# Optimization experiments

Measured on AMD Instinct MI355X. Metric: run time of the kernel, lower is better.

## Reference

```python
import jax, jax.numpy as jnp
import numpy as np

N_NODES = 50000
N_EDGES = 800000
VOCAB = 4096
EMB = 128
HID = 128


def glorot(key, shape):
    limit = float(np.sqrt(6.0 / (shape[0] + shape[1])))
    return jax.random.uniform(key, shape, jnp.float32, -limit, limit)


def setup_inputs() -> dict:
    key = jax.random.key(0)
    k = jax.random.split(key, 6)
    x = jax.random.randint(k[0], (N_NODES, 1), 0, VOCAB, dtype=jnp.int64)
    edge_index = jax.random.randint(k[1], (2, N_EDGES), 0, N_NODES, dtype=jnp.int64)
    # Embedding init: normal(0, dim^-0.5)
    emb = jax.random.normal(k[2], (VOCAB, EMB), jnp.float32) * (EMB ** -0.5)
    W1 = glorot(k[3], (EMB, 2 * HID))
    b1 = jnp.zeros((2 * HID,), jnp.float32)
    W2 = glorot(k[4], (2 * HID, HID))
    b2 = jnp.zeros((HID,), jnp.float32)
    return {"x": x, "edge_index": edge_index, "emb": emb,
            "W1": W1, "b1": b1, "W2": W2, "b2": b2}


def _gcn_conv(h, src, dst, norm, W, b):
    # PyG GCNConv: transform then degree-normalized aggregate over A + I.
    h = h @ W                                   # [N, F_out]
    msg = norm[:, None] * h[src]                # [(E+N), F_out] gather
    out = jax.ops.segment_sum(msg, dst, num_segments=N_NODES)  # scatter-add
    return out + b


def _edges_with_self_loops_and_norm(edge_index):
    loop = jnp.arange(N_NODES, dtype=edge_index.dtype)
    src = jnp.concatenate([edge_index[0], loop])
    dst = jnp.concatenate([edge_index[1], loop])
    deg = jax.ops.segment_sum(jnp.ones_like(dst, jnp.float32), dst,
                              num_segments=N_NODES)
    inv_sqrt = jnp.where(deg > 0, deg ** -0.5, 0.0)
    norm = inv_sqrt[src] * inv_sqrt[dst]        # [(E+N)]
    return src, dst, norm


def reference(x, edge_index, emb, W1, b1, W2, b2):
    src, dst, norm = _edges_with_self_loops_and_norm(edge_index)
    h = emb[x[:, 0]]                            # embedding lookup + squeeze(1)
    h = jax.nn.relu(_gcn_conv(h, src, dst, norm, W1, b1))
    h = _gcn_conv(h, src, dst, norm, W2, b2)
    return h
```

## Files before the change

kernel.cpp:

```cpp
#include <hip/hip_runtime.h>


constexpr int FEAT = 128;
constexpr int HID2 = 256;
constexpr int CAP  = 64;

typedef __attribute__((ext_vector_type(8))) __bf16 bf16x8;
typedef __attribute__((ext_vector_type(4))) float f32x4;
typedef __attribute__((ext_vector_type(8))) _Float16 f16x8;
union FragU { uint4 u; bf16x8 b; };
union H16 { _Float16 f; unsigned short u; };

__device__ inline void split_bf16_rne(float v, unsigned short& h, unsigned short& l) {
  unsigned u = __float_as_uint(v);
  unsigned short hh = (unsigned short)((u + 0x7FFFu + ((u >> 16) & 1u)) >> 16);
  float r = v - __uint_as_float(((unsigned)hh) << 16);
  unsigned u2 = __float_as_uint(r);
  unsigned short ll = (unsigned short)((u2 + 0x7FFFu + ((u2 >> 16) & 1u)) >> 16);
  h = hh; l = ll;
}

__device__ inline void split_trunc1(float v, unsigned short& h, unsigned short& l) {
  unsigned u = __float_as_uint(v);
  h = (unsigned short)(u >> 16);
  float r = v - __uint_as_float(u & 0xFFFF0000u);
  l = (unsigned short)(__float_as_uint(r) >> 16);
}


__global__ __launch_bounds__(256) void k_init_prep(int* cnt, int N, int nblkN,
    const float* __restrict__ W1, const float* __restrict__ W2,
    unsigned short* __restrict__ w1s_hi, unsigned short* __restrict__ w1s_lo,
    unsigned short* __restrict__ w2s_hi, unsigned short* __restrict__ w2s_lo) {
  int b = blockIdx.x;
  if (b < nblkN) {
    int i = b * 256 + threadIdx.x;
    if (i < N) cnt[i] = 0;
    return;
  }
  int idx = (b - nblkN) * 256 + threadIdx.x;
  unsigned short h, l;
  if (idx < FEAT * HID2) {
    int k = idx >> 8, n = idx & 255;
    split_bf16_rne(W1[idx], h, l);
    int t = n >> 4, lr = n & 15, kc = k >> 5, quad = (k >> 3) & 3, j = k & 7;
    int us = (((t * 4 + kc) * 64 + quad * 16 + lr) << 3) + j;
    w1s_hi[us] = h;
    w1s_lo[us] = l;
  } else {
    int jj = idx - FEAT * HID2;
    int k = jj >> 7, n = jj & 127;
    split_bf16_rne(W2[jj], h, l);
    int t = n >> 4, lr = n & 15, kc = k >> 5, quad = (k >> 3) & 3, j = k & 7;
    int us = (((t * 8 + kc) * 64 + quad * 16 + lr) << 3) + j;
    w2s_hi[us] = h;
    w2s_lo[us] = l;
  }
}


__global__ __launch_bounds__(256) void k_bucket(const int* __restrict__ src,
    const int* __restrict__ dst, int* cnt, unsigned short* csr, int E, int chunkN) {
  int g = blockIdx.x & 7;
  int e = (blockIdx.x >> 3) * 256 + threadIdx.x;
  if (e >= E) return;
  int d = dst[e];
  int lo = g * chunkN;
  if (d >= lo && d < lo + chunkN) {
    int pos = atomicAdd(&cnt[d], 1);
    if (pos < CAP) csr[d * CAP + pos] = (unsigned short)src[e];
  }
}


__global__ __launch_bounds__(256, 3) void k_gmlp(
    const int* __restrict__ x, const float* __restrict__ emb,
    const int* __restrict__ cnt, const unsigned short* __restrict__ csr,
    const uint4* __restrict__ w1s_hi, const uint4* __restrict__ w1s_lo,
    const uint4* __restrict__ w2s_hi, const uint4* __restrict__ w2s_lo,
    const float* __restrict__ b1,
    unsigned short* __restrict__ hs2h, int N, int Np) {
  __shared__ __align__(16) unsigned short aggh[2 * 4 * 64 * 8];
  __shared__ __align__(16) unsigned short aggl[2 * 4 * 64 * 8];
  __shared__ __align__(16) unsigned short h1h[32 * 256];
  __shared__ __align__(16) unsigned short h1l[32 * 256];

  int tid  = threadIdx.x;
  int wave = tid >> 6, lane = tid & 63, quad = lane >> 4, lr = lane & 15;
  int bid  = blockIdx.x;
  int m0 = bid * 32;
  int rot1 = bid & 3;
  int ti0  = bid & 1;
  int kh0  = (bid >> 1) & 1;

  int glr = tid >> 4;
  int c4  = (tid & 15) * 4;
  int kcg = c4 >> 5, qdg = (c4 >> 3) & 3, sub = c4 & 7;

  #pragma unroll
  for (int g = 0; g < 2; ++g) {
    int node = m0 + g * 16 + glr;
    int usA = (((g * 4 + kcg) * 64 + qdg * 16 + glr) << 3) + sub;
    int usB = (((g * 4 + kcg + 2) * 64 + qdg * 16 + glr) << 3) + sub;
    if (node < N) {
      int degN = cnt[node];
      float wd = rsqrtf((float)(degN + 1));
      int deg = degN > CAP ? CAP : degN;

      const float* e0 = &emb[(long long)x[node] * FEAT + c4];
      float4 aA = *reinterpret_cast<const float4*>(e0);
      float4 aB = *reinterpret_cast<const float4*>(e0 + 64);
      aA.x *= wd; aA.y *= wd; aA.z *= wd; aA.w *= wd;
      aB.x *= wd; aB.y *= wd; aB.z *= wd; aB.w *= wd;

      const unsigned short* row = csr + node * CAP;
      int j = 0;
      for (; j + 7 < deg; j += 8) {
        uint4 c8 = *reinterpret_cast<const uint4*>(row + j);
        int s[8] = {(int)(c8.x & 0xFFFF), (int)(c8.x >> 16),
                    (int)(c8.y & 0xFFFF), (int)(c8.y >> 16),
                    (int)(c8.z & 0xFFFF), (int)(c8.z >> 16),
                    (int)(c8.w & 0xFFFF), (int)(c8.w >> 16)};
        const float* p[8];
        #pragma unroll
        for (int q = 0; q < 8; ++q) p[q] = &emb[(long long)x[s[q]] * FEAT + c4];
        float ws[8];
        #pragma unroll
        for (int q = 0; q < 8; ++q) ws[q] = rsqrtf((float)(cnt[s[q]] + 1));
        float4 rA[8], rB[8];
        #pragma unroll
        for (int q = 0; q < 8; ++q) {
          rA[q] = *reinterpret_cast<const float4*>(p[q]);
          rB[q] = *reinterpret_cast<const float4*>(p[q] + 64);
        }
        #pragma unroll
        for (int q = 0; q < 8; ++q) {
          aA.x += ws[q] * rA[q].x; aA.y += ws[q] * rA[q].y;
          aA.z += ws[q] * rA[q].z; aA.w += ws[q] * rA[q].w;
          aB.x += ws[q] * rB[q].x; aB.y += ws[q] * rB[q].y;
          aB.z += ws[q] * rB[q].z; aB.w += ws[q] * rB[q].w;
        }
      }
      if (j + 3 < deg) {
        uint2 c4e = *reinterpret_cast<const uint2*>(row + j);
        int s[4] = {(int)(c4e.x & 0xFFFF), (int)(c4e.x >> 16),
                    (int)(c4e.y & 0xFFFF), (int)(c4e.y >> 16)};
        const float* p[4];
        #pragma unroll
        for (int q = 0; q < 4; ++q) p[q] = &emb[(long long)x[s[q]] * FEAT + c4];
        float ws[4];
        #pragma unroll
        for (int q = 0; q < 4; ++q) ws[q] = rsqrtf((float)(cnt[s[q]] + 1));
        float4 rA[4], rB[4];
        #pragma unroll
        for (int q = 0; q < 4; ++q) {
          rA[q] = *reinterpret_cast<const float4*>(p[q]);
          rB[q] = *reinterpret_cast<const float4*>(p[q] + 64);
        }
        #pragma unroll
        for (int q = 0; q < 4; ++q) {
          aA.x += ws[q] * rA[q].x; aA.y += ws[q] * rA[q].y;
          aA.z += ws[q] * rA[q].z; aA.w += ws[q] * rA[q].w;
          aB.x += ws[q] * rB[q].x; aB.y += ws[q] * rB[q].y;
          aB.z += ws[q] * rB[q].z; aB.w += ws[q] * rB[q].w;
        }
        j += 4;
      }
      for (; j < deg; ++j) {
        int s = row[j];
        float w = rsqrtf((float)(cnt[s] + 1));
        const float* p = &emb[(long long)x[s] * FEAT + c4];
        float4 a = *reinterpret_cast<const float4*>(p);
        float4 b = *reinterpret_cast<const float4*>(p + 64);
        aA.x += w * a.x; aA.y += w * a.y; aA.z += w * a.z; aA.w += w * a.w;
        aB.x += w * b.x; aB.y += w * b.y; aB.z += w * b.z; aB.w += w * b.w;
      }

      aA.x *= wd; aA.y *= wd; aA.z *= wd; aA.w *= wd;
      aB.x *= wd; aB.y *= wd; aB.z *= wd; aB.w *= wd;
      ushort4 hA, lA, hB, lB;
      split_bf16_rne(aA.x, hA.x, lA.x);
      split_bf16_rne(aA.y, hA.y, lA.y);
      split_bf16_rne(aA.z, hA.z, lA.z);
      split_bf16_rne(aA.w, hA.w, lA.w);
      split_bf16_rne(aB.x, hB.x, lB.x);
      split_bf16_rne(aB.y, hB.y, lB.y);
      split_bf16_rne(aB.z, hB.z, lB.z);
      split_bf16_rne(aB.w, hB.w, lB.w);
      *reinterpret_cast<ushort4*>(aggh + usA) = hA;
      *reinterpret_cast<ushort4*>(aggl + usA) = lA;
      *reinterpret_cast<ushort4*>(aggh + usB) = hB;
      *reinterpret_cast<ushort4*>(aggl + usB) = lB;
    } else {
      ushort4 z = {0, 0, 0, 0};
      *reinterpret_cast<ushort4*>(aggh + usA) = z;
      *reinterpret_cast<ushort4*>(aggl + usA) = z;
      *reinterpret_cast<ushort4*>(aggh + usB) = z;
      *reinterpret_cast<ushort4*>(aggl + usB) = z;
    }
  }

  FragU bh[2][4], bl[2][4];
  auto loadB1 = [&](int t, int buf) {
    #pragma unroll
    for (int kc = 0; kc < 4; ++kc) {
      bh[buf][kc].u = w1s_hi[(t * 4 + kc) * 64 + lane];
      bl[buf][kc].u = w1s_lo[(t * 4 + kc) * 64 + lane];
    }
  };
  int t0 = wave * 4;
  loadB1(t0 + rot1, 0);

  __syncthreads();

  FragU a1h[2][4], a1l[2][4];
  #pragma unroll
  for (int rt = 0; rt < 2; ++rt)
    #pragma unroll
    for (int kc = 0; kc < 4; ++kc) {
      int us = ((rt * 4 + kc) * 64 + lane) << 3;
      a1h[rt][kc].u = *reinterpret_cast<const uint4*>(aggh + us);
      a1l[rt][kc].u = *reinterpret_cast<const uint4*>(aggl + us);
    }

  auto comp1 = [&](int t, int buf) {
    f32x4 hh[2], hl[2], lh[2];
    #pragma unroll
    for (int rt = 0; rt < 2; ++rt) {
      hh[rt] = f32x4{0.f, 0.f, 0.f, 0.f};
      hl[rt] = f32x4{0.f, 0.f, 0.f, 0.f};
      lh[rt] = f32x4{0.f, 0.f, 0.f, 0.f};
    }
    #pragma unroll
    for (int kc = 0; kc < 4; ++kc)
      #pragma unroll
      for (int rt = 0; rt < 2; ++rt) {
        hh[rt] = __builtin_amdgcn_mfma_f32_16x16x32_bf16(a1h[rt][kc].b, bh[buf][kc].b, hh[rt], 0, 0, 0);
        hl[rt] = __builtin_amdgcn_mfma_f32_16x16x32_bf16(a1h[rt][kc].b, bl[buf][kc].b, hl[rt], 0, 0, 0);
        lh[rt] = __builtin_amdgcn_mfma_f32_16x16x32_bf16(a1l[rt][kc].b, bh[buf][kc].b, lh[rt], 0, 0, 0);
      }
    float bias = b1[t * 16 + lr];
    int c = t * 2 + (lr >> 3), jj = lr & 7;
    #pragma unroll
    for (int rt = 0; rt < 2; ++rt)
      #pragma unroll
      for (int r = 0; r < 4; ++r) {
        float v = hh[rt][r] + hl[rt][r] + lh[rt][r] + bias;
        v = v > 0.f ? v : 0.f;
        int row = rt * 16 + quad * 4 + r;
        int us = ((row * 32 + (c ^ (row & 7))) << 3) + jj;
        unsigned short sh, sl;
        split_trunc1(v, sh, sl);
        h1h[us] = sh;
        h1l[us] = sl;
      }
  };

  #pragma unroll
  for (int i = 0; i < 4; ++i) {
    if (i < 3) loadB1(t0 + ((i + 1 + rot1) & 3), (i + 1) & 1);
    comp1(t0 + ((i + rot1) & 3), i & 1);
  }

  float inv_r[2][4];
  #pragma unroll
  for (int rt = 0; rt < 2; ++rt)
    #pragma unroll
    for (int r = 0; r < 4; ++r) {
      int gg = m0 + rt * 16 + quad * 4 + r;
      inv_r[rt][r] = rsqrtf((float)(cnt[gg < N ? gg : N - 1] + 1));
    }

  FragU pb2h[4], pb2l[4];
  {
    int t2p = wave * 2 + ti0;
    #pragma unroll
    for (int kc = 0; kc < 4; ++kc) {
      pb2h[kc].u = w2s_hi[(t2p * 8 + kh0 * 4 + kc) * 64 + lane];
      pb2l[kc].u = w2s_lo[(t2p * 8 + kh0 * 4 + kc) * 64 + lane];
    }
  }

  __syncthreads();

  #pragma unroll
  for (int tii = 0; tii < 2; ++tii) {
    int ti = ti0 ^ tii;
    int t2 = wave * 2 + ti;
    f32x4 hh[2], hl[2], lh[2];
    #pragma unroll
    for (int rt = 0; rt < 2; ++rt) {
      hh[rt] = f32x4{0.f, 0.f, 0.f, 0.f};
      hl[rt] = f32x4{0.f, 0.f, 0.f, 0.f};
      lh[rt] = f32x4{0.f, 0.f, 0.f, 0.f};
    }
    #pragma unroll
    for (int khi = 0; khi < 2; ++khi) {
      int kh = kh0 ^ khi;
      FragU b2h[4], b2l[4];
      if (tii == 0 && khi == 0) {
        #pragma unroll
        for (int kc = 0; kc < 4; ++kc) { b2h[kc] = pb2h[kc]; b2l[kc] = pb2l[kc]; }
      } else {
        #pragma unroll
        for (int kc = 0; kc < 4; ++kc) {
          b2h[kc].u = w2s_hi[(t2 * 8 + kh * 4 + kc) * 64 + lane];
          b2l[kc].u = w2s_lo[(t2 * 8 + kh * 4 + kc) * 64 + lane];
        }
      }
      FragU a2h[2][4], a2l[2][4];
      #pragma unroll
      for (int rt = 0; rt < 2; ++rt) {
        int row = rt * 16 + lr;
        #pragma unroll
        for (int kc = 0; kc < 4; ++kc) {
          int pc = (kh * 16 + kc * 4 + quad) ^ (row & 7);
          a2h[rt][kc].u = *reinterpret_cast<const uint4*>(&h1h[(row * 32 + pc) << 3]);
          a2l[rt][kc].u = *reinterpret_cast<const uint4*>(&h1l[(row * 32 + pc) << 3]);
        }
      }
      #pragma unroll
      for (int kc = 0; kc < 4; ++kc)
        #pragma unroll
        for (int rt = 0; rt < 2; ++rt) {
          hh[rt] = __builtin_amdgcn_mfma_f32_16x16x32_bf16(a2h[rt][kc].b, b2h[kc].b, hh[rt], 0, 0, 0);
          hl[rt] = __builtin_amdgcn_mfma_f32_16x16x32_bf16(a2h[rt][kc].b, b2l[kc].b, hl[rt], 0, 0, 0);
          lh[rt] = __builtin_amdgcn_mfma_f32_16x16x32_bf16(a2l[rt][kc].b, b2h[kc].b, lh[rt], 0, 0, 0);
        }
    }
    unsigned short* sl2 = hs2h + (long long)(t2 >> 2) * Np * 64 + (t2 & 3) * 16;
    #pragma unroll
    for (int rt = 0; rt < 2; ++rt)
      #pragma unroll
      for (int r = 0; r < 4; ++r) {
        int gg = m0 + rt * 16 + quad * 4 + r;
        if (gg < N) {
          float v = (hh[rt][r] + hl[rt][r] + lh[rt][r]) * inv_r[rt][r];
          H16 cv;
          cv.f = (_Float16)v;
          sl2[(long long)gg * 64 + lr] = cv.u;
        }
      }
  }
}


__global__ __launch_bounds__(256) void k_gather_l2(
    const unsigned short* __restrict__ hs2h,
    const int* __restrict__ cnt, const unsigned short* __restrict__ csr,
    const float* __restrict__ bias, float* __restrict__ out, int N, int Np) {
  int g    = blockIdx.x & 7;
  int half = g >> 2, qtr = g & 3;
  int Nq   = (N + 3) >> 2;
  int local = (blockIdx.x >> 3) * 32 + (threadIdx.x >> 3);
  if (local >= Nq) return;
  int node = qtr * Nq + local;
  if (node >= N) return;
  int f8 = (threadIdx.x & 7) * 8;
  const unsigned short* sl = hs2h + (long long)half * Np * 64;

  f32x4 a0, a1;
  {
    f16x8 v = *reinterpret_cast<const f16x8*>(sl + (long long)node * 64 + f8);
    a0 = __builtin_convertvector(__builtin_shufflevector(v, v, 0, 1, 2, 3), f32x4);
    a1 = __builtin_convertvector(__builtin_shufflevector(v, v, 4, 5, 6, 7), f32x4);
  }

  const unsigned short* row = csr + node * CAP;
  int degN = cnt[node];
  int deg = degN > CAP ? CAP : degN;
  int j = 0;
  for (; j + 15 < deg; j += 16) {
    uint4 c0 = *reinterpret_cast<const uint4*>(row + j);
    uint4 c1 = *reinterpret_cast<const uint4*>(row + j + 8);
    int s[16] = {(int)(c0.x & 0xFFFF), (int)(c0.x >> 16),
                 (int)(c0.y & 0xFFFF), (int)(c0.y >> 16),
                 (int)(c0.z & 0xFFFF), (int)(c0.z >> 16),
                 (int)(c0.w & 0xFFFF), (int)(c0.w >> 16),
                 (int)(c1.x & 0xFFFF), (int)(c1.x >> 16),
                 (int)(c1.y & 0xFFFF), (int)(c1.y >> 16),
                 (int)(c1.z & 0xFFFF), (int)(c1.z >> 16),
                 (int)(c1.w & 0xFFFF), (int)(c1.w >> 16)};
    f16x8 r[16];
    #pragma unroll
    for (int q = 0; q < 16; ++q)
      r[q] = *reinterpret_cast<const f16x8*>(sl + (long long)s[q] * 64 + f8);
    #pragma unroll
    for (int q = 0; q < 16; ++q) {
      a0 += __builtin_convertvector(__builtin_shufflevector(r[q], r[q], 0, 1, 2, 3), f32x4);
      a1 += __builtin_convertvector(__builtin_shufflevector(r[q], r[q], 4, 5, 6, 7), f32x4);
    }
  }
  if (j + 7 < deg) {
    uint4 c8 = *reinterpret_cast<const uint4*>(row + j);
    int s[8] = {(int)(c8.x & 0xFFFF), (int)(c8.x >> 16),
                (int)(c8.y & 0xFFFF), (int)(c8.y >> 16),
                (int)(c8.z & 0xFFFF), (int)(c8.z >> 16),
                (int)(c8.w & 0xFFFF), (int)(c8.w >> 16)};
    f16x8 r[8];
    #pragma unroll
    for (int q = 0; q < 8; ++q)
      r[q] = *reinterpret_cast<const f16x8*>(sl + (long long)s[q] * 64 + f8);
    #pragma unroll
    for (int q = 0; q < 8; ++q) {
      a0 += __builtin_convertvector(__builtin_shufflevector(r[q], r[q], 0, 1, 2, 3), f32x4);
      a1 += __builtin_convertvector(__builtin_shufflevector(r[q], r[q], 4, 5, 6, 7), f32x4);
    }
    j += 8;
  }
  if (j + 3 < deg) {
    uint2 c4e = *reinterpret_cast<const uint2*>(row + j);
    int s[4] = {(int)(c4e.x & 0xFFFF), (int)(c4e.x >> 16),
                (int)(c4e.y & 0xFFFF), (int)(c4e.y >> 16)};
    f16x8 r[4];
    #pragma unroll
    for (int q = 0; q < 4; ++q)
      r[q] = *reinterpret_cast<const f16x8*>(sl + (long long)s[q] * 64 + f8);
    #pragma unroll
    for (int q = 0; q < 4; ++q) {
      a0 += __builtin_convertvector(__builtin_shufflevector(r[q], r[q], 0, 1, 2, 3), f32x4);
      a1 += __builtin_convertvector(__builtin_shufflevector(r[q], r[q], 4, 5, 6, 7), f32x4);
    }
    j += 4;
  }
  for (; j < deg; ++j) {
    f16x8 v = *reinterpret_cast<const f16x8*>(sl + (long long)row[j] * 64 + f8);
    a0 += __builtin_convertvector(__builtin_shufflevector(v, v, 0, 1, 2, 3), f32x4);
    a1 += __builtin_convertvector(__builtin_shufflevector(v, v, 4, 5, 6, 7), f32x4);
  }

  float w = rsqrtf((float)(degN + 1));
  int col = half * 64 + f8;
  f32x4 b0 = *reinterpret_cast<const f32x4*>(&bias[col]);
  f32x4 b1v = *reinterpret_cast<const f32x4*>(&bias[col + 4]);
  a0 = a0 * w + b0;
  a1 = a1 * w + b1v;
  *reinterpret_cast<f32x4*>(&out[(long long)node * FEAT + col]) = a0;
  *reinterpret_cast<f32x4*>(&out[(long long)node * FEAT + col + 4]) = a1;
}


extern "C" void kernel_launch(void* const* d_in, const int* in_sizes, int n_in,
                              void* d_out, int out_size, void* d_ws, size_t ws_size,
                              hipStream_t stream) {
  const int*   x   = (const int*)d_in[0];
  const int*   ei  = (const int*)d_in[1];
  const float* emb = (const float*)d_in[2];
  const float* W1  = (const float*)d_in[3];
  const float* b1  = (const float*)d_in[4];
  const float* W2  = (const float*)d_in[5];
  const float* b2  = (const float*)d_in[6];
  float* out = (float*)d_out;

  const int N  = in_sizes[0];
  const int E  = in_sizes[1] / 2;
  const int nblk_mlp = (N + 31) / 32;
  const int Np = nblk_mlp * 32;
  const int chunkN = (N + 7) / 8;
  const int* src = ei;
  const int* dst = ei + E;

  int* cnt = (int*)d_ws;
  unsigned short* csr = (unsigned short*)(cnt + N);
  unsigned short* hs2h = csr + (long long)N * CAP;
  unsigned short* w1s_hi = hs2h + (long long)Np * FEAT;
  unsigned short* w1s_lo = w1s_hi + FEAT * HID2;
  unsigned short* w2s_hi = w1s_lo + FEAT * HID2;
  unsigned short* w2s_lo = w2s_hi + FEAT * HID2;

  const int Nq = (N + 3) / 4;
  const int nblk_N  = (N + 255) / 256;
  const int nblk_E8 = ((E + 255) / 256) * 8;
  const int nblk_g2 = ((Nq + 31) / 32) * 8;

  k_init_prep<<<nblk_N + 256, 256, 0, stream>>>(cnt, N, nblk_N, W1, W2,
                                                w1s_hi, w1s_lo, w2s_hi, w2s_lo);
  k_bucket<<<nblk_E8, 256, 0, stream>>>(src, dst, cnt, csr, E, chunkN);

  k_gmlp<<<nblk_mlp, 256, 0, stream>>>(x, emb, cnt, csr,
                                       (const uint4*)w1s_hi, (const uint4*)w1s_lo,
                                       (const uint4*)w2s_hi, (const uint4*)w2s_lo,
                                       b1, hs2h, N, Np);
  k_gather_l2<<<nblk_g2, 256, 0, stream>>>(hs2h, cnt, csr, b2, out, N, Np);
}
```

Before: 212.9 us.

## Swizzle LDS aggregate layout, batch neighbor gathers by 16, regroup layer-2 gather threads

Applies an XOR swizzle to the shared-memory aggregate buffers on both the write and MFMA-fragment read sides to reduce LDS bank conflicts. Replaces the 8/4/1 tiered neighbor loop in layer-1 aggregation with a 16-wide padded loop that masks tail entries with zero weight, so more independent loads are in flight. The layer-2 gather now has both feature halves of a node handled by adjacent threads within one block instead of separate blocks, changing the node-to-block mapping. The padded loop issues redundant loads for the tail entries and reads up to 16 csr entries, possibly past the valid degree but within the CAP row.

```diff
diff --git a/kernel.cpp b/kernel.cpp
--- a/kernel.cpp
+++ b/kernel.cpp
@@ -96,12 +96,16 @@
   int glr = tid >> 4;
   int c4  = (tid & 15) * 4;
   int kcg = c4 >> 5, qdg = (c4 >> 3) & 3, sub = c4 & 7;
+  int L   = qdg * 16 + glr;
+  int posL = L ^ ((L >> 4) & 3);
 
   #pragma unroll
   for (int g = 0; g < 2; ++g) {
     int node = m0 + g * 16 + glr;
-    int usA = (((g * 4 + kcg) * 64 + qdg * 16 + glr) << 3) + sub;
-    int usB = (((g * 4 + kcg + 2) * 64 + qdg * 16 + glr) << 3) + sub;
+    int fA = g * 4 + kcg, fB = fA + 2;
+    int pos = posL ^ ((fA & 1) << 2);
+    int usA = ((fA * 64 + pos) << 3) + sub;
+    int usB = ((fB * 64 + pos) << 3) + sub;
     if (node < N) {
       int degN = cnt[node];
       float wd = rsqrtf((float)(degN + 1));
@@ -114,66 +118,51 @@
       aB.x *= wd; aB.y *= wd; aB.z *= wd; aB.w *= wd;
 
       const unsigned short* row = csr + node * CAP;
-      int j = 0;
-      for (; j + 7 < deg; j += 8) {
-        uint4 c8 = *reinterpret_cast<const uint4*>(row + j);
-        int s[8] = {(int)(c8.x & 0xFFFF), (int)(c8.x >> 16),
-                    (int)(c8.y & 0xFFFF), (int)(c8.y >> 16),
-                    (int)(c8.z & 0xFFFF), (int)(c8.z >> 16),
-                    (int)(c8.w & 0xFFFF), (int)(c8.w >> 16)};
-        const float* p[8];
-        #pragma unroll
-        for (int q = 0; q < 8; ++q) p[q] = &emb[(long long)x[s[q]] * FEAT + c4];
-        float ws[8];
-        #pragma unroll
-        for (int q = 0; q < 8; ++q) ws[q] = rsqrtf((float)(cnt[s[q]] + 1));
-        float4 rA[8], rB[8];
-        #pragma unroll
-        for (int q = 0; q < 8; ++q) {
-          rA[q] = *reinterpret_cast<const float4*>(p[q]);
-          rB[q] = *reinterpret_cast<const float4*>(p[q] + 64);
-        }
-        #pragma unroll
-        for (int q = 0; q < 8; ++q) {
-          aA.x += ws[q] * rA[q].x; aA.y += ws[q] * rA[q].y;
-          aA.z += ws[q] * rA[q].z; aA.w += ws[q] * rA[q].w;
-          aB.x += ws[q] * rB[q].x; aB.y += ws[q] * rB[q].y;
-          aB.z += ws[q] * rB[q].z; aB.w += ws[q] * rB[q].w;
-        }
-      }
-      if (j + 3 < deg) {
-        uint2 c4e = *reinterpret_cast<const uint2*>(row + j);
-        int s[4] = {(int)(c4e.x & 0xFFFF), (int)(c4e.x >> 16),
-                    (int)(c4e.y & 0xFFFF), (int)(c4e.y >> 16)};
-        const float* p[4];
-        #pragma unroll
-        for (int q = 0; q < 4; ++q) p[q] = &emb[(long long)x[s[q]] * FEAT + c4];
-        float ws[4];
-        #pragma unroll
-        for (int q = 0; q < 4; ++q) ws[q] = rsqrtf((float)(cnt[s[q]] + 1));
-        float4 rA[4], rB[4];
-        #pragma unroll
-        for (int q = 0; q < 4; ++q) {
-          rA[q] = *reinterpret_cast<const float4*>(p[q]);
-          rB[q] = *reinterpret_cast<const float4*>(p[q] + 64);
-        }
-        #pragma unroll
-        for (int q = 0; q < 4; ++q) {
-          aA.x += ws[q] * rA[q].x; aA.y += ws[q] * rA[q].y;
-          aA.z += ws[q] * rA[q].z; aA.w += ws[q] * rA[q].w;
-          aB.x += ws[q] * rB[q].x; aB.y += ws[q] * rB[q].y;
-          aB.z += ws[q] * rB[q].z; aB.w += ws[q] * rB[q].w;
-        }
-        j += 4;
-      }
-      for (; j < deg; ++j) {
-        int s = row[j];
-        float w = rsqrtf((float)(cnt[s] + 1));
-        const float* p = &emb[(long long)x[s] * FEAT + c4];
-        float4 a = *reinterpret_cast<const float4*>(p);
-        float4 b = *reinterpret_cast<const float4*>(p + 64);
-        aA.x += w * a.x; aA.y += w * a.y; aA.z += w * a.z; aA.w += w * a.w;
-        aB.x += w * b.x; aB.y += w * b.y; aB.z += w * b.z; aB.w += w * b.w;
+      for (int j = 0; j < deg; j += 16) {
+        int nrem = deg - j;
+        uint4 c0 = *reinterpret_cast<const uint4*>(row + j);
+        uint4 c1 = *reinterpret_cast<const uint4*>(row + j + 8);
+        int s[16] = {(int)(c0.x & 0xFFFF), (int)(c0.x >> 16),
+                     (int)(c0.y & 0xFFFF), (int)(c0.y >> 16),
+                     (int)(c0.z & 0xFFFF), (int)(c0.z >> 16),
+                     (int)(c0.w & 0xFFFF), (int)(c0.w >> 16),
+                     (int)(c1.x & 0xFFFF), (int)(c1.x >> 16),
+                     (int)(c1.y & 0xFFFF), (int)(c1.y >> 16),
+                     (int)(c1.z & 0xFFFF), (int)(c1.z >> 16),
+                     (int)(c1.w & 0xFFFF), (int)(c1.w >> 16)};
+        #pragma unroll
+        for (int q = 0; q < 16; ++q)
+          if (q >= nrem) s[q] = s[0];
+        int xs[16];
+        #pragma unroll
+        for (int q = 0; q < 16; ++q) xs[q] = x[s[q]];
+        float ws[16];
+        #pragma unroll
+        for (int q = 0; q < 16; ++q) {
+          float w = rsqrtf((float)(cnt[s[q]] + 1));
+          ws[q] = q < nrem ? w : 0.0f;
+        }
+        #pragma unroll
+        for (int h = 0; h < 2; ++h) {
+          const float* p[8];
+          #pragma unroll
+          for (int q = 0; q < 8; ++q)
+            p[q] = &emb[(long long)xs[h * 8 + q] * FEAT + c4];
+          float4 rA[8], rB[8];
+          #pragma unroll
+          for (int q = 0; q < 8; ++q) {
+            rA[q] = *reinterpret_cast<const float4*>(p[q]);
+            rB[q] = *reinterpret_cast<const float4*>(p[q] + 64);
+          }
+          #pragma unroll
+          for (int q = 0; q < 8; ++q) {
+            float w = ws[h * 8 + q];
+            aA.x += w * rA[q].x; aA.y += w * rA[q].y;
+            aA.z += w * rA[q].z; aA.w += w * rA[q].w;
+            aB.x += w * rB[q].x; aB.y += w * rB[q].y;
+            aB.z += w * rB[q].z; aB.w += w * rB[q].w;
+          }
+        }
       }
 
       aA.x *= wd; aA.y *= wd; aA.z *= wd; aA.w *= wd;
@@ -214,14 +203,18 @@
   __syncthreads();
 
   FragU a1h[2][4], a1l[2][4];
-  #pragma unroll
-  for (int rt = 0; rt < 2; ++rt)
-    #pragma unroll
-    for (int kc = 0; kc < 4; ++kc) {
-      int us = ((rt * 4 + kc) * 64 + lane) << 3;
-      a1h[rt][kc].u = *reinterpret_cast<const uint4*>(aggh + us);
-      a1l[rt][kc].u = *reinterpret_cast<const uint4*>(aggl + us);
-    }
+  {
+    int posR = lane ^ ((lane >> 4) & 3);
+    #pragma unroll
+    for (int rt = 0; rt < 2; ++rt)
+      #pragma unroll
+      for (int kc = 0; kc < 4; ++kc) {
+        int f = rt * 4 + kc;
+        int us = ((f * 64 + (posR ^ ((f & 1) << 2))) << 3);
+        a1h[rt][kc].u = *reinterpret_cast<const uint4*>(aggh + us);
+        a1l[rt][kc].u = *reinterpret_cast<const uint4*>(aggl + us);
+      }
+  }
 
   auto comp1 = [&](int t, int buf) {
     f32x4 hh[2], hl[2], lh[2];
@@ -349,14 +342,14 @@
     const unsigned short* __restrict__ hs2h,
     const int* __restrict__ cnt, const unsigned short* __restrict__ csr,
     const float* __restrict__ bias, float* __restrict__ out, int N, int Np) {
-  int g    = blockIdx.x & 7;
-  int half = g >> 2, qtr = g & 3;
-  int Nq   = (N + 3) >> 2;
-  int local = (blockIdx.x >> 3) * 32 + (threadIdx.x >> 3);
-  if (local >= Nq) return;
-  int node = qtr * Nq + local;
+  int oct  = blockIdx.x & 7;
+  int No   = (N + 7) >> 3;
+  int local = (blockIdx.x >> 3) * 16 + (threadIdx.x >> 4);
+  if (local >= No) return;
+  int node = oct * No + local;
   if (node >= N) return;
-  int f8 = (threadIdx.x & 7) * 8;
+  int half = (threadIdx.x >> 3) & 1;
+  int f8   = (threadIdx.x & 7) * 8;
   const unsigned short* sl = hs2h + (long long)half * Np * 64;
 
   f32x4 a0, a1;
@@ -468,10 +461,10 @@
   unsigned short* w2s_hi = w1s_lo + FEAT * HID2;
   unsigned short* w2s_lo = w2s_hi + FEAT * HID2;
 
-  const int Nq = (N + 3) / 4;
+  const int No = (N + 7) / 8;
   const int nblk_N  = (N + 255) / 256;
   const int nblk_E8 = ((E + 255) / 256) * 8;
-  const int nblk_g2 = ((Nq + 31) / 32) * 8;
+  const int nblk_g2 = ((No + 15) / 16) * 8;
 
   k_init_prep<<<nblk_N + 256, 256, 0, stream>>>(cnt, N, nblk_N, W1, W2,
                                                 w1s_hi, w1s_lo, w2s_hi, w2s_lo);
```

Measured after the change: 248.5 us. +16.7%, slower.
